# Optimization experiments

Hardware: AMD Instinct MI355X
Metric: run time of the kernel (lower is better)

## Reference

```python
import jax, jax.numpy as jnp
import numpy as np

K = 3          # kernel size
PAD = 1        # (K-1)//2, stride=1, dilation=1


def _modulated_deform_conv(depth, offset, mask, w, b):
    """torchvision deform_conv2d with in_ch=out_ch=1, stride=1, pad=1, dil=1.
    depth:  [B,1,H,W]
    offset: [B,2*K*K,H,W]  interleaved (dy, dx) per kernel tap
    mask:   [B,K*K,H,W]    modulation scalars
    w:      [1,1,K,K]      conv weights (ones buffer)
    b:      [1]            bias (zeros buffer)
    """
    B, _, H, W = depth.shape
    kk = K * K
    img = depth[:, 0]                                    # [B,H,W]

    off = offset.reshape(B, kk, 2, H, W)
    dy, dx = off[:, :, 0], off[:, :, 1]                  # [B,kk,H,W]

    # integer tap offsets of the 3x3 kernel
    ky, kx = jnp.meshgrid(jnp.arange(K), jnp.arange(K), indexing='ij')
    ky = ky.reshape(kk).astype(depth.dtype)
    kx = kx.reshape(kk).astype(depth.dtype)

    iy = jnp.arange(H, dtype=depth.dtype)
    ix = jnp.arange(W, dtype=depth.dtype)
    # sampling coords per output pixel per tap: [B,kk,H,W]
    y = iy[None, None, :, None] - PAD + ky[None, :, None, None] + dy
    x = ix[None, None, None, :] - PAD + kx[None, :, None, None] + dx

    y0f = jnp.floor(y); x0f = jnp.floor(x)
    wy = y - y0f; wx = x - x0f                           # frac parts
    y0 = y0f.astype(jnp.int32); x0 = x0f.astype(jnp.int32)
    y1 = y0 + 1;  x1 = x0 + 1

    bidx = jnp.arange(B)[:, None, None, None]

    def corner(yc, xc):
        inb = (yc >= 0) & (yc < H) & (xc >= 0) & (xc < W)
        v = img[bidx, jnp.clip(yc, 0, H - 1), jnp.clip(xc, 0, W - 1)]
        return jnp.where(inb, v, jnp.zeros((), depth.dtype))

    sampled = (corner(y0, x0) * (1 - wy) * (1 - wx)
             + corner(y0, x1) * (1 - wy) * wx
             + corner(y1, x0) * wy * (1 - wx)
             + corner(y1, x1) * wy * wx)                 # [B,kk,H,W]

    wk = w.reshape(1, kk, 1, 1)
    out = jnp.sum(sampled * mask * wk, axis=1) + b[0]    # [B,H,W]
    return out[:, None]                                  # [B,1,H,W]


def setup_inputs() -> dict:
    key = jax.random.key(0)
    k1, k2, k3 = jax.random.split(key, 3)
    B, H, W = 8, 512, 512
    depth  = jax.random.normal(k1, (B, 1, H, W), dtype=jnp.float32)
    weight = jax.random.uniform(k2, (B, K * K, H, W), dtype=jnp.float32)
    offset = jax.random.normal(k3, (B, 2 * K * K, H, W), dtype=jnp.float32)
    w = jnp.ones((1, 1, K, K), dtype=jnp.float32)   # buffer 'w'
    b = jnp.zeros((1,), dtype=jnp.float32)          # buffer 'b'
    return {"depth": depth, "weight": weight, "offset": offset, "w": w, "b": b}


def reference(depth, weight, offset, w, b):
    return _modulated_deform_conv(depth, offset, weight, w, b)
```

## Files before the change

### kernel.cpp

```cpp
#include <hip/hip_runtime.h>


#define KK 9
#define PAD 1
#define H 512
#define W 512
#define HW (H * W)

#define TX 64
#define TY 16
#define HALO 8
#define LWL (TX + 2 * HALO)
#define LH  (TY + 2 * HALO)
#define LWS 84
#define NCHUNK (LH * LWL / 4)
#define SAFE ((LH - 2) * LWS + (LWL - 2))
#define TRASH (LH * LWS)

typedef float f2 __attribute__((ext_vector_type(2)));
typedef float f4 __attribute__((ext_vector_type(4)));

__device__ __forceinline__ float bilin_global(const float* __restrict__ img,
                                              float y, float x) {
    float y0f = floorf(y);
    float x0f = floorf(x);
    int y0 = (int)y0f;
    int x0 = (int)x0f;
    float wy = y - y0f;
    float wx = x - x0f;
    int y1 = y0 + 1;
    int x1 = x0 + 1;

    bool y0i = (y0 >= 0) & (y0 < H);
    bool y1i = (y1 >= 0) & (y1 < H);
    bool x0i = (x0 >= 0) & (x0 < W);
    bool x1i = (x1 >= 0) & (x1 < W);

    int y0c = min(max(y0, 0), H - 1);
    int y1c = min(max(y1, 0), H - 1);
    int x0c = min(max(x0, 0), W - 1);
    int x1c = min(max(x1, 0), W - 1);

    float v00 = (y0i & x0i) ? img[y0c * W + x0c] : 0.0f;
    float v01 = (y0i & x1i) ? img[y0c * W + x1c] : 0.0f;
    float v10 = (y1i & x0i) ? img[y1c * W + x0c] : 0.0f;
    float v11 = (y1i & x1i) ? img[y1c * W + x1c] : 0.0f;

    float omwy = 1.0f - wy;
    float omwx = 1.0f - wx;
    return fmaf(v00 * omwy, omwx,
           fmaf(v01 * omwy, wx,
           fmaf(v10 * wy,   omwx, v11 * wy * wx)));
}

__device__ __forceinline__ float sample_nb(const float* S, float syr, float sxr,
                                           int& oob) {
    const float y0f = floorf(syr);
    const float x0f = floorf(sxr);
    const float wy = syr - y0f;
    const float wx = sxr - x0f;
    const int ly = (int)y0f;
    const int lx = (int)x0f;
    oob |= (int)(((unsigned)ly >= (unsigned)(LH - 1)) |
                 ((unsigned)lx >= (unsigned)(LWL - 1)));
    unsigned su = (unsigned)(ly * LWS + lx);
    su = su < (unsigned)SAFE ? su : (unsigned)SAFE;
    const float v00 = S[su];
    const float v01 = S[su + 1];
    const float v10 = S[su + LWS];
    const float v11 = S[su + LWS + 1];
    const float omwy = 1.0f - wy;
    const float omwx = 1.0f - wx;
    return fmaf(v00 * omwy, omwx,
           fmaf(v01 * omwy, wx,
           fmaf(v10 * wy,   omwx, v11 * wy * wx)));
}

__global__ __launch_bounds__(256, 4) void dcn_kernel(
    const float* __restrict__ depth,
    const float* __restrict__ mask,
    const float* __restrict__ offset,
    const float* __restrict__ w9,
    const float* __restrict__ bias,
    float* __restrict__ out) {
    __shared__ float S[LH * LWS + 4];

    const int b  = blockIdx.z;
    const int bx = blockIdx.x;
    const int by = blockIdx.y;
    const int tX0 = bx * TX - HALO;
    const int tY0 = by * TY - HALO;

    const float* __restrict__ img = depth + (long)b * HW;

    const int xq = threadIdx.x & 15;
    const int yr = threadIdx.x >> 4;
    const int tx = bx * TX + 4 * xq;
    const int ty = by * TY + yr;
    const int pix = ty * W + tx;

    const float* __restrict__ msk = mask   + ((long)b * KK)     * HW + pix;
    const float* __restrict__ off = offset + ((long)b * 2 * KK) * HW + pix;

    const float wk0 = w9[0], wk1 = w9[1], wk2 = w9[2];
    const float wk3 = w9[3], wk4 = w9[4], wk5 = w9[5];
    const float wk6 = w9[6], wk7 = w9[7], wk8 = w9[8];
    const float bs = bias[0];

    f4 dy0, dy1, dy2, dy3, dy4, dy5, dy6, dy7, dy8;
    f4 dx0, dx1, dx2, dx3, dx4, dx5, dx6, dx7, dx8;
    f4 m0, m1, m2, m3, m4, m5, m6, m7, m8;
#define LDT(k)                                              \
    dy##k = *(const f4*)(off + (2 * k) * HW);               \
    dx##k = *(const f4*)(off + (2 * k + 1) * HW);           \
    m##k  = *(const f4*)(msk + k * HW);
    LDT(0) LDT(1) LDT(2) LDT(3) LDT(4) LDT(5) LDT(6) LDT(7) LDT(8)
#undef LDT

    #pragma unroll
    for (int j = 0; j < 3; ++j) {
        const int c   = (int)threadIdx.x + j * 256;
        const int ly  = c / 20;
        const int lx4 = (c - ly * 20) * 4;
        const int gy  = tY0 + ly;
        const int gx  = tX0 + lx4;
        const int ok  = (int)(((unsigned)gy < (unsigned)H) &
                              ((unsigned)gx < (unsigned)W));
        const f4 v = *(const f4*)(img + (ok ? (gy * W + gx) : 0));
        f4 z;
        z.x = ok ? v.x : 0.0f;
        z.y = ok ? v.y : 0.0f;
        z.z = ok ? v.z : 0.0f;
        z.w = ok ? v.w : 0.0f;
        const int si = (c < NCHUNK) ? (ly * LWS + lx4) : TRASH;
        *(f4*)(S + si) = z;
    }
    __syncthreads();

    float a0 = bs, a1 = bs, a2 = bs, a3 = bs;
    int oob = 0;
    const float sybr = (float)(yr + HALO - PAD);
    const float sxbr = (float)(4 * xq + HALO - PAD);

#define CTAP(k, KYC, KXC, WK)                                                  \
    {                                                                          \
        const float syk = sybr + (float)(KYC);                                 \
        const float sxk = sxbr + (float)(KXC);                                 \
        a0 = fmaf(sample_nb(S, syk + dy##k.x, sxk + 0.0f + dx##k.x, oob),      \
                  m##k.x * (WK), a0);                                          \
        a1 = fmaf(sample_nb(S, syk + dy##k.y, sxk + 1.0f + dx##k.y, oob),      \
                  m##k.y * (WK), a1);                                          \
        a2 = fmaf(sample_nb(S, syk + dy##k.z, sxk + 2.0f + dx##k.z, oob),      \
                  m##k.z * (WK), a2);                                          \
        a3 = fmaf(sample_nb(S, syk + dy##k.w, sxk + 3.0f + dx##k.w, oob),      \
                  m##k.w * (WK), a3);                                          \
    }
    CTAP(0, 0, 0, wk0) CTAP(1, 0, 1, wk1) CTAP(2, 0, 2, wk2)
    CTAP(3, 1, 0, wk3) CTAP(4, 1, 1, wk4) CTAP(5, 1, 2, wk5)
    CTAP(6, 2, 0, wk6) CTAP(7, 2, 1, wk7) CTAP(8, 2, 2, wk8)
#undef CTAP

    if (__builtin_expect(__any(oob), 0)) {
        if (oob) {
            a0 = bs; a1 = bs; a2 = bs; a3 = bs;
#pragma unroll 1
            for (int k = 0; k < KK; ++k) {
                const int ky = k / 3;
                const int kx = k - 3 * ky;
                const float wk = w9[k];
                const float syb = (float)(ty - PAD + ky);
                const float sxb = (float)(tx - PAD + kx);
#pragma unroll 1
                for (int p = 0; p < 4; ++p) {
                    const float fdy = off[(2 * k) * HW + p];
                    const float fdx = off[(2 * k + 1) * HW + p];
                    const float fm  = msk[k * HW + p];
                    const float sv  = bilin_global(img, syb + fdy,
                                                   sxb + (float)p + fdx);
                    const float add = sv * fm * wk;
                    a0 += (p == 0) ? add : 0.0f;
                    a1 += (p == 1) ? add : 0.0f;
                    a2 += (p == 2) ? add : 0.0f;
                    a3 += (p == 3) ? add : 0.0f;
                }
            }
        }
    }

    f4 r;
    r.x = a0; r.y = a1; r.z = a2; r.w = a3;
    *(f4*)(out + (long)b * HW + pix) = r;
}

extern "C" void kernel_launch(void* const* d_in, const int* in_sizes, int n_in,
                              void* d_out, int out_size, void* d_ws, size_t ws_size,
                              hipStream_t stream) {
    const float* depth  = (const float*)d_in[0];
    const float* mask   = (const float*)d_in[1];
    const float* offset = (const float*)d_in[2];
    const float* w9     = (const float*)d_in[3];
    const float* bias   = (const float*)d_in[4];
    float* out = (float*)d_out;

    const int B = in_sizes[0] / HW;

    dim3 block(256);
    dim3 grid(W / TX, H / TY, B);
    dcn_kernel<<<grid, block, 0, stream>>>(depth, mask, offset, w9, bias, out);
}
```

Before: 280.6 us.

## Stage offsets and masks into LDS via async global_load_lds, one pixel per thread

Replaces per-thread f4 register loads of the 27 offset/mask planes with asynchronous global-to-LDS direct loads, so each thread handles a single pixel and reads its taps from shared memory. The tile shrinks to 32x8 with the same 8-pixel halo, and the launch-bounds occupancy hint rises from 4 to 5 blocks. The aim is to cut register pressure and overlap the offset/mask streaming with the depth tile fill. In exchange the halo-to-output ratio rises sharply, so each block loads more redundant depth data, and the vector stores become scalar.

```diff
diff --git a/kernel.cpp b/kernel.cpp
--- a/kernel.cpp
+++ b/kernel.cpp
@@ -7,18 +7,26 @@
 #define W 512
 #define HW (H * W)
 
-#define TX 64
-#define TY 16
+#define TX 32
+#define TY 8
 #define HALO 8
 #define LWL (TX + 2 * HALO)
 #define LH  (TY + 2 * HALO)
-#define LWS 84
-#define NCHUNK (LH * LWL / 4)
-#define SAFE ((LH - 2) * LWS + (LWL - 2))
-#define TRASH (LH * LWS)
-
-typedef float f2 __attribute__((ext_vector_type(2)));
+#define TILE_N (LH * LWL)
+#define NCHUNK (TILE_N / 4)
+#define SAFE ((LH - 2) * LWL + (LWL - 2))
+#define NPL 27
+#define PL_FLOATS (NPL * 256)
+#define TILE_OFF PL_FLOATS
+#define TRASH (TILE_OFF + TILE_N)
+
 typedef float f4 __attribute__((ext_vector_type(4)));
+
+__device__ __forceinline__ void async_ld4(const float* g, float* l) {
+    __builtin_amdgcn_global_load_lds(
+        (const __attribute__((address_space(1))) void*)g,
+        (__attribute__((address_space(3))) void*)l, 4, 0, 0);
+}
 
 __device__ __forceinline__ float bilin_global(const float* __restrict__ img,
                                               float y, float x) {
@@ -53,7 +61,7 @@
            fmaf(v10 * wy,   omwx, v11 * wy * wx)));
 }
 
-__device__ __forceinline__ float sample_nb(const float* S, float syr, float sxr,
+__device__ __forceinline__ float sample_nb(const float* T, float syr, float sxr,
                                            int& oob) {
     const float y0f = floorf(syr);
     const float x0f = floorf(sxr);
@@ -63,12 +71,12 @@
     const int lx = (int)x0f;
     oob |= (int)(((unsigned)ly >= (unsigned)(LH - 1)) |
                  ((unsigned)lx >= (unsigned)(LWL - 1)));
-    unsigned su = (unsigned)(ly * LWS + lx);
+    unsigned su = (unsigned)(ly * LWL + lx);
     su = su < (unsigned)SAFE ? su : (unsigned)SAFE;
-    const float v00 = S[su];
-    const float v01 = S[su + 1];
-    const float v10 = S[su + LWS];
-    const float v11 = S[su + LWS + 1];
+    const float v00 = T[su];
+    const float v01 = T[su + 1];
+    const float v10 = T[su + LWL];
+    const float v11 = T[su + LWL + 1];
     const float omwy = 1.0f - wy;
     const float omwx = 1.0f - wx;
     return fmaf(v00 * omwy, omwx,
@@ -76,14 +84,14 @@
            fmaf(v10 * wy,   omwx, v11 * wy * wx)));
 }
 
-__global__ __launch_bounds__(256, 4) void dcn_kernel(
+__global__ __launch_bounds__(256, 5) void dcn_kernel(
     const float* __restrict__ depth,
     const float* __restrict__ mask,
     const float* __restrict__ offset,
     const float* __restrict__ w9,
     const float* __restrict__ bias,
     float* __restrict__ out) {
-    __shared__ float S[LH * LWS + 4];
+    __shared__ float LDSb[PL_FLOATS + TILE_N + 4];
 
     const int b  = blockIdx.z;
     const int bx = blockIdx.x;
@@ -93,35 +101,32 @@
 
     const float* __restrict__ img = depth + (long)b * HW;
 
-    const int xq = threadIdx.x & 15;
-    const int yr = threadIdx.x >> 4;
-    const int tx = bx * TX + 4 * xq;
+    const int tid = (int)threadIdx.x;
+    const int xc = tid & 31;
+    const int yr = tid >> 5;
+    const int tx = bx * TX + xc;
     const int ty = by * TY + yr;
     const int pix = ty * W + tx;
 
-    const float* __restrict__ msk = mask   + ((long)b * KK)     * HW + pix;
-    const float* __restrict__ off = offset + ((long)b * 2 * KK) * HW + pix;
-
-    const float wk0 = w9[0], wk1 = w9[1], wk2 = w9[2];
-    const float wk3 = w9[3], wk4 = w9[4], wk5 = w9[5];
-    const float wk6 = w9[6], wk7 = w9[7], wk8 = w9[8];
-    const float bs = bias[0];
-
-    f4 dy0, dy1, dy2, dy3, dy4, dy5, dy6, dy7, dy8;
-    f4 dx0, dx1, dx2, dx3, dx4, dx5, dx6, dx7, dx8;
-    f4 m0, m1, m2, m3, m4, m5, m6, m7, m8;
-#define LDT(k)                                              \
-    dy##k = *(const f4*)(off + (2 * k) * HW);               \
-    dx##k = *(const f4*)(off + (2 * k + 1) * HW);           \
-    m##k  = *(const f4*)(msk + k * HW);
-    LDT(0) LDT(1) LDT(2) LDT(3) LDT(4) LDT(5) LDT(6) LDT(7) LDT(8)
-#undef LDT
-
+    const float* __restrict__ offp = offset + ((long)b * 2 * KK) * HW + pix;
+    const float* __restrict__ mskp = mask   + ((long)b * KK)     * HW + pix;
+
+    {
+        float* pl = LDSb + (tid >> 6) * 64;
+        #pragma unroll
+        for (int j = 0; j < 18; ++j)
+            async_ld4(offp + j * HW, pl + j * 256);
+        #pragma unroll
+        for (int j = 0; j < 9; ++j)
+            async_ld4(mskp + j * HW, pl + (18 + j) * 256);
+    }
+
+    float* T = LDSb + TILE_OFF;
     #pragma unroll
-    for (int j = 0; j < 3; ++j) {
-        const int c   = (int)threadIdx.x + j * 256;
-        const int ly  = c / 20;
-        const int lx4 = (c - ly * 20) * 4;
+    for (int j = 0; j < 2; ++j) {
+        const int c   = tid + j * 256;
+        const int ly  = c / 12;
+        const int lx4 = (c - ly * 12) * 4;
         const int gy  = tY0 + ly;
         const int gx  = tX0 + lx4;
         const int ok  = (int)(((unsigned)gy < (unsigned)H) &
@@ -132,28 +137,30 @@
         z.y = ok ? v.y : 0.0f;
         z.z = ok ? v.z : 0.0f;
         z.w = ok ? v.w : 0.0f;
-        const int si = (c < NCHUNK) ? (ly * LWS + lx4) : TRASH;
-        *(f4*)(S + si) = z;
-    }
+        const int si = (c < NCHUNK) ? (TILE_OFF + ly * LWL + lx4) : TRASH;
+        *(f4*)(LDSb + si) = z;
+    }
+
     __syncthreads();
 
-    float a0 = bs, a1 = bs, a2 = bs, a3 = bs;
+    const float wk0 = w9[0], wk1 = w9[1], wk2 = w9[2];
+    const float wk3 = w9[3], wk4 = w9[4], wk5 = w9[5];
+    const float wk6 = w9[6], wk7 = w9[7], wk8 = w9[8];
+    const float bs = bias[0];
+
+    float acc = bs;
     int oob = 0;
     const float sybr = (float)(yr + HALO - PAD);
-    const float sxbr = (float)(4 * xq + HALO - PAD);
+    const float sxbr = (float)(xc + HALO - PAD);
 
 #define CTAP(k, KYC, KXC, WK)                                                  \
     {                                                                          \
-        const float syk = sybr + (float)(KYC);                                 \
-        const float sxk = sxbr + (float)(KXC);                                 \
-        a0 = fmaf(sample_nb(S, syk + dy##k.x, sxk + 0.0f + dx##k.x, oob),      \
-                  m##k.x * (WK), a0);                                          \
-        a1 = fmaf(sample_nb(S, syk + dy##k.y, sxk + 1.0f + dx##k.y, oob),      \
-                  m##k.y * (WK), a1);                                          \
-        a2 = fmaf(sample_nb(S, syk + dy##k.z, sxk + 2.0f + dx##k.z, oob),      \
-                  m##k.z * (WK), a2);                                          \
-        a3 = fmaf(sample_nb(S, syk + dy##k.w, sxk + 3.0f + dx##k.w, oob),      \
-                  m##k.w * (WK), a3);                                          \
+        const float dyk = LDSb[(2 * (k)) * 256 + tid];                         \
+        const float dxk = LDSb[(2 * (k) + 1) * 256 + tid];                     \
+        const float mk  = LDSb[(18 + (k)) * 256 + tid];                        \
+        const float sy = sybr + (float)(KYC) + dyk;                            \
+        const float sx = sxbr + (float)(KXC) + dxk;                            \
+        acc = fmaf(sample_nb(T, sy, sx, oob), mk * (WK), acc);                 \
     }
     CTAP(0, 0, 0, wk0) CTAP(1, 0, 1, wk1) CTAP(2, 0, 2, wk2)
     CTAP(3, 1, 0, wk3) CTAP(4, 1, 1, wk4) CTAP(5, 1, 2, wk5)
@@ -162,34 +169,23 @@
 
     if (__builtin_expect(__any(oob), 0)) {
         if (oob) {
-            a0 = bs; a1 = bs; a2 = bs; a3 = bs;
+            acc = bs;
 #pragma unroll 1
             for (int k = 0; k < KK; ++k) {
                 const int ky = k / 3;
                 const int kx = k - 3 * ky;
                 const float wk = w9[k];
-                const float syb = (float)(ty - PAD + ky);
-                const float sxb = (float)(tx - PAD + kx);
-#pragma unroll 1
-                for (int p = 0; p < 4; ++p) {
-                    const float fdy = off[(2 * k) * HW + p];
-                    const float fdx = off[(2 * k + 1) * HW + p];
-                    const float fm  = msk[k * HW + p];
-                    const float sv  = bilin_global(img, syb + fdy,
-                                                   sxb + (float)p + fdx);
-                    const float add = sv * fm * wk;
-                    a0 += (p == 0) ? add : 0.0f;
-                    a1 += (p == 1) ? add : 0.0f;
-                    a2 += (p == 2) ? add : 0.0f;
-                    a3 += (p == 3) ? add : 0.0f;
-                }
+                const float fdy = offp[(2 * k) * HW];
+                const float fdx = offp[(2 * k + 1) * HW];
+                const float fm  = mskp[k * HW];
+                const float sy = (float)(ty - PAD + ky) + fdy;
+                const float sx = (float)(tx - PAD + kx) + fdx;
+                acc = fmaf(bilin_global(img, sy, sx), fm * wk, acc);
             }
         }
     }
 
-    f4 r;
-    r.x = a0; r.y = a1; r.z = a2; r.w = a3;
-    *(f4*)(out + (long)b * HW + pix) = r;
+    out[(long)b * HW + pix] = acc;
 }
 
 extern "C" void kernel_launch(void* const* d_in, const int* in_sizes, int n_in,
```

Measured after the change: 277.9 us. Within noise of the previous version (-1.0%).
